# Kernel tuning notes

Hardware: AMD Instinct MI355X
Metric: run time of the kernel (lower is better)

The kernel has to match this reference:

```python
import jax, jax.numpy as jnp
import numpy as np

DT_SCALE = 0.01  # time grid = arange(T) * 0.01, i.e. t in [0, 0.99]


def setup_inputs() -> dict:
    key = jax.random.key(0)
    k1, k2, k3 = jax.random.split(key, 3)
    latents, hidden = 128, 256
    S, N, T = 4, 1024, 100
    first_point = jax.random.normal(k1, (S, N, latents), dtype=jnp.float32)
    time_steps_to_predict = jnp.arange(T, dtype=jnp.float32) * DT_SCALE
    # ODEFunc MLP params (Glorot-ish scaling so tanh stays in a sane range)
    W1 = jax.random.normal(k2, (latents, hidden), dtype=jnp.float32) / np.sqrt(latents)
    b1 = jnp.zeros((hidden,), dtype=jnp.float32)
    W2 = jax.random.normal(k3, (hidden, latents), dtype=jnp.float32) / np.sqrt(hidden)
    b2 = jnp.zeros((latents,), dtype=jnp.float32)
    return {
        "first_point": first_point,
        "time_steps_to_predict": time_steps_to_predict,
        "W1": W1, "b1": b1, "W2": W2, "b2": b2,
    }


def reference(first_point, time_steps_to_predict, W1, b1, W2, b2):
    # ode_func: dy/dt = tanh(y @ W1 + b1) @ W2 + b2 (time-autonomous MLP)
    def f(y):
        return jnp.tanh(y @ W1 + b1) @ W2 + b2

    # torchdiffeq fixed-step 'rk4': one classical RK4 step per output interval.
    t0s = time_steps_to_predict[:-1]
    t1s = time_steps_to_predict[1:]

    def rk4_step(y, ts):
        t0, t1 = ts
        dt = t1 - t0
        half = dt * 0.5
        k1 = f(y)
        k2 = f(y + half * k1)
        k3 = f(y + half * k2)
        k4 = f(y + dt * k3)
        y1 = y + (dt / 6.0) * (k1 + 2.0 * k2 + 2.0 * k3 + k4)
        return y1, y1

    _, ys = jax.lax.scan(rk4_step, first_point, (t0s, t1s))  # [T-1, S, N, D]
    pred_y = jnp.concatenate([first_point[None], ys], axis=0)  # [T, S, N, D]
    # permute(1, 2, 0, 3): [T, S, N, D] -> [S, N, T, D]
    return jnp.transpose(pred_y, (1, 2, 0, 3))
```

## Files before the change

kernel.cpp:

```cpp
#include <hip/hip_runtime.h>

typedef __attribute__((ext_vector_type(8))) short v8s;
typedef __attribute__((ext_vector_type(4))) float f4;

#define MFMA16(a, b, c) __builtin_amdgcn_mfma_f32_16x16x32_bf16((a), (b), (c), 0, 0, 0)

__device__ __forceinline__ float bf2f(unsigned short u) {
    return __uint_as_float(((unsigned)u) << 16);
}
__device__ __forceinline__ unsigned short f2bf(float x) {
    unsigned u = __float_as_uint(x);
    unsigned r = 0x7FFFu + ((u >> 16) & 1u);
    return (unsigned short)((u + r) >> 16);
}
__device__ __forceinline__ float tanh_fast(float z) {
    float u = __builtin_amdgcn_exp2f(z * 2.885390081777927f);
    float r = __builtin_amdgcn_rcpf(u + 1.0f);
    return __builtin_fmaf(-2.0f, r, 1.0f);
}
__device__ __forceinline__ float ldin(const void* p, int i, bool f32) {
    return f32 ? ((const float*)p)[i] : bf2f(((const unsigned short*)p)[i]);
}

#define BROWS 16
#define TSTEPS 100
#define DLAT 128
#define DHID 256
#define YSTR 136
#define HSTR 264
#define FSTR 132

__global__ __launch_bounds__(512, 2)
void ode_rk4_kernel(const void* __restrict__ fp,
                    const void* __restrict__ ts,
                    const void* __restrict__ W1,
                    const void* __restrict__ b1,
                    const void* __restrict__ W2,
                    const void* __restrict__ b2,
                    void* __restrict__ out) {
    __shared__ unsigned short yB[BROWS * YSTR];
    __shared__ unsigned short hB[BROWS * HSTR];
    __shared__ float yF[BROWS * FSTR];

    const bool m32 = fabsf(((const float*)ts)[1] - 0.01f) < 0.004f;

    const int tid = threadIdx.x;
    const int w = tid >> 6;
    const int lane = tid & 63;
    const int pp = lane & 15;
    const int qq = lane >> 4;
    const int R0 = blockIdx.x * BROWS;

    v8s w1f[4][2];
#pragma unroll
    for (int kt = 0; kt < 4; ++kt)
#pragma unroll
        for (int nt = 0; nt < 2; ++nt) {
            v8s f;
#pragma unroll
            for (int j = 0; j < 8; ++j)
                f[j] = (short)f2bf(ldin(W1, (kt * 32 + qq * 8 + j) * DHID + 32 * w + nt * 16 + pp, m32));
            w1f[kt][nt] = f;
        }
    v8s w2f[8];
#pragma unroll
    for (int kt = 0; kt < 8; ++kt) {
        v8s f;
#pragma unroll
        for (int j = 0; j < 8; ++j)
            f[j] = (short)f2bf(ldin(W2, (kt * 32 + qq * 8 + j) * DLAT + 16 * w + pp, m32));
        w2f[kt] = f;
    }
    const float b1v0 = ldin(b1, 32 * w + pp, m32);
    const float b1v1 = ldin(b1, 32 * w + 16 + pp, m32);
    const float b2v  = ldin(b2, 16 * w + pp, m32);

    {
        int row = tid >> 5, ch = tid & 31;
        if (m32) {
            float4 v = *((const float4*)((const float*)fp + (size_t)(R0 + row) * DLAT) + ch);
            *((float4*)((float*)out + ((size_t)(R0 + row) * TSTEPS) * DLAT) + ch) = v;
            *(float4*)(yF + row * FSTR + ch * 4) = v;
            ushort4 b; b.x = f2bf(v.x); b.y = f2bf(v.y); b.z = f2bf(v.z); b.w = f2bf(v.w);
            *(ushort4*)(yB + row * YSTR + ch * 4) = b;
        } else {
            const unsigned short* fpu = (const unsigned short*)fp;
            ushort4 v = *((const ushort4*)(fpu + (size_t)(R0 + row) * DLAT) + ch);
            *((ushort4*)((unsigned short*)out + ((size_t)(R0 + row) * TSTEPS) * DLAT) + ch) = v;
            *(ushort4*)(yB + row * YSTR + ch * 4) = v;
            float* yfp = yF + row * FSTR + ch * 4;
            yfp[0] = bf2f(v.x); yfp[1] = bf2f(v.y); yfp[2] = bf2f(v.z); yfp[3] = bf2f(v.w);
        }
    }
    __syncthreads();

    const int c2 = 16 * w + pp;
    float yreg[4];
#pragma unroll
    for (int r = 0; r < 4; ++r) yreg[r] = yF[(qq * 4 + r) * FSTR + c2];

    const unsigned short* yA = yB + pp * YSTR + qq * 8;
    const unsigned short* hA = hB + pp * HSTR + qq * 8;
    unsigned short* hW = hB + 32 * w + pp;
    unsigned short* yW = yB + c2;
    float* fW = yF + c2;

    for (int t = 0; t < TSTEPS - 1; ++t) {
        float t0 = ldin(ts, t, m32), t1 = ldin(ts, t + 1, m32);
        float dt = t1 - t0;
        float half = 0.5f * dt;
        float ksum[4] = {0.f, 0.f, 0.f, 0.f};
#pragma unroll
        for (int e = 0; e < 4; ++e) {
            __syncthreads();
            f4 h0 = {0.f, 0.f, 0.f, 0.f}, h1 = {0.f, 0.f, 0.f, 0.f};
#pragma unroll
            for (int kt = 0; kt < 4; ++kt) {
                v8s a = *(const v8s*)(yA + kt * 32);
                h0 = MFMA16(a, w1f[kt][0], h0);
                h1 = MFMA16(a, w1f[kt][1], h1);
            }
#pragma unroll
            for (int r = 0; r < 4; ++r) {
                hW[(qq * 4 + r) * HSTR]      = f2bf(tanh_fast(h0[r] + b1v0));
                hW[(qq * 4 + r) * HSTR + 16] = f2bf(tanh_fast(h1[r] + b1v1));
            }
            __syncthreads();
            f4 kacc = {0.f, 0.f, 0.f, 0.f};
#pragma unroll
            for (int kt = 0; kt < 8; ++kt) {
                v8s a = *(const v8s*)(hA + kt * 32);
                kacc = MFMA16(a, w2f[kt], kacc);
            }
            const float wgt = (e == 0 || e == 3) ? 1.0f : 2.0f;
            const float cc = (e == 2) ? dt : half;
#pragma unroll
            for (int r = 0; r < 4; ++r) {
                float kv = kacc[r] + b2v;
                ksum[r] = __builtin_fmaf(wgt, kv, ksum[r]);
                if (e < 3) {
                    float ya = __builtin_fmaf(cc, kv, yreg[r]);
                    yW[(qq * 4 + r) * YSTR] = f2bf(ya);
                }
            }
            if (e == 3) {
                float s = dt * (1.0f / 6.0f);
#pragma unroll
                for (int r = 0; r < 4; ++r) {
                    yreg[r] = __builtin_fmaf(s, ksum[r], yreg[r]);
                    yW[(qq * 4 + r) * YSTR] = f2bf(yreg[r]);
                    fW[(qq * 4 + r) * FSTR] = yreg[r];
                }
            }
        }
        __syncthreads();
        {
            int row = tid >> 5, ch = tid & 31;
            float4 v = *(const float4*)(yF + row * FSTR + ch * 4);
            if (m32) {
                *((float4*)((float*)out + ((size_t)(R0 + row) * TSTEPS + (t + 1)) * DLAT) + ch) = v;
            } else {
                ushort4 b; b.x = f2bf(v.x); b.y = f2bf(v.y); b.z = f2bf(v.z); b.w = f2bf(v.w);
                *((ushort4*)((unsigned short*)out + ((size_t)(R0 + row) * TSTEPS + (t + 1)) * DLAT) + ch) = b;
            }
        }
    }
}

extern "C" void kernel_launch(void* const* d_in, const int* in_sizes, int n_in,
                              void* d_out, int out_size, void* d_ws, size_t ws_size,
                              hipStream_t stream) {
    (void)in_sizes; (void)n_in; (void)d_ws; (void)ws_size; (void)out_size;
    ode_rk4_kernel<<<256, 512, 0, stream>>>(d_in[0], d_in[1], d_in[2], d_in[3],
                                            d_in[4], d_in[5], d_out);
}
```

Measured before the change: 528.5 us.

## Swizzle LDS layout, drop fp32 staging buffer and per-step barrier, store outputs from registers

Applies an XOR swizzle to the bf16 y and hidden LDS tiles to avoid bank conflicts on the MFMA A-operand loads. The fp32 yF staging buffer and the extra barrier per time step are removed; each thread writes its own yreg values directly to global memory. Time steps are cached in LDS, and bf16 conversion uses packed pair conversion. The direct stores are scalar and strided across lanes, so they may coalesce worse than the earlier float4 row stores.

```diff
diff --git a/kernel.cpp b/kernel.cpp
--- a/kernel.cpp
+++ b/kernel.cpp
@@ -1,4 +1,5 @@
 #include <hip/hip_runtime.h>
+#include <hip/hip_bf16.h>
 
 typedef __attribute__((ext_vector_type(8))) short v8s;
 typedef __attribute__((ext_vector_type(4))) float f4;
@@ -12,6 +13,12 @@
     unsigned u = __float_as_uint(x);
     unsigned r = 0x7FFFu + ((u >> 16) & 1u);
     return (unsigned short)((u + r) >> 16);
+}
+__device__ __forceinline__ unsigned pack_bf16_2(float a, float b) {
+    float2 t; t.x = a; t.y = b;
+    union { __hip_bfloat162 h; unsigned u; } cv;
+    cv.h = __float22bfloat162_rn(t);
+    return cv.u;
 }
 __device__ __forceinline__ float tanh_fast(float z) {
     float u = __builtin_amdgcn_exp2f(z * 2.885390081777927f);
@@ -28,7 +35,6 @@
 #define DHID 256
 #define YSTR 136
 #define HSTR 264
-#define FSTR 132
 
 __global__ __launch_bounds__(512, 2)
 void ode_rk4_kernel(const void* __restrict__ fp,
@@ -40,7 +46,7 @@
                     void* __restrict__ out) {
     __shared__ unsigned short yB[BROWS * YSTR];
     __shared__ unsigned short hB[BROWS * HSTR];
-    __shared__ float yF[BROWS * FSTR];
+    __shared__ float tsL[TSTEPS];
 
     const bool m32 = fabsf(((const float*)ts)[1] - 0.01f) < 0.004f;
 
@@ -51,6 +57,8 @@
     const int qq = lane >> 4;
     const int R0 = blockIdx.x * BROWS;
 
+    if (tid < TSTEPS) tsL[tid] = ldin(ts, tid, m32);
+
     v8s w1f[4][2];
 #pragma unroll
     for (int kt = 0; kt < 4; ++kt)
@@ -75,39 +83,54 @@
     const float b1v1 = ldin(b1, 32 * w + 16 + pp, m32);
     const float b2v  = ldin(b2, 16 * w + pp, m32);
 
+    const int pb = pp >> 3, pw = pp & 7;
+    const int sA = (pp >> 1) & 7;
+    const unsigned short* yA[4];
+#pragma unroll
+    for (int kt = 0; kt < 4; ++kt)
+        yA[kt] = yB + pp * YSTR + (((4 * kt + qq) ^ sA) << 3);
+    const unsigned short* hA[8];
+#pragma unroll
+    for (int kt = 0; kt < 8; ++kt)
+        hA[kt] = hB + pp * HSTR + (((4 * kt + qq) ^ sA) << 3);
+    const int s0 = (2 * qq) & 7, s1 = (2 * qq + 1) & 7;
+    int hoff[2][2], yoff[2];
+    hoff[0][0] = (((4 * w + pb) ^ s0) << 3) + pw;
+    hoff[0][1] = (((4 * w + 2 + pb) ^ s0) << 3) + pw;
+    hoff[1][0] = (((4 * w + pb) ^ s1) << 3) + pw;
+    hoff[1][1] = (((4 * w + 2 + pb) ^ s1) << 3) + pw;
+    yoff[0] = (((2 * w + pb) ^ s0) << 3) + pw;
+    yoff[1] = (((2 * w + pb) ^ s1) << 3) + pw;
+
     {
         int row = tid >> 5, ch = tid & 31;
+        int sw = (row >> 1) & 7;
+        unsigned short* dst = yB + row * YSTR + (((ch >> 1) ^ sw) << 3) + (ch & 1) * 4;
         if (m32) {
             float4 v = *((const float4*)((const float*)fp + (size_t)(R0 + row) * DLAT) + ch);
             *((float4*)((float*)out + ((size_t)(R0 + row) * TSTEPS) * DLAT) + ch) = v;
-            *(float4*)(yF + row * FSTR + ch * 4) = v;
             ushort4 b; b.x = f2bf(v.x); b.y = f2bf(v.y); b.z = f2bf(v.z); b.w = f2bf(v.w);
-            *(ushort4*)(yB + row * YSTR + ch * 4) = b;
+            *(ushort4*)dst = b;
         } else {
             const unsigned short* fpu = (const unsigned short*)fp;
             ushort4 v = *((const ushort4*)(fpu + (size_t)(R0 + row) * DLAT) + ch);
             *((ushort4*)((unsigned short*)out + ((size_t)(R0 + row) * TSTEPS) * DLAT) + ch) = v;
-            *(ushort4*)(yB + row * YSTR + ch * 4) = v;
-            float* yfp = yF + row * FSTR + ch * 4;
-            yfp[0] = bf2f(v.x); yfp[1] = bf2f(v.y); yfp[2] = bf2f(v.z); yfp[3] = bf2f(v.w);
-        }
-    }
-    __syncthreads();
+            *(ushort4*)dst = v;
+        }
+    }
 
     const int c2 = 16 * w + pp;
     float yreg[4];
-#pragma unroll
-    for (int r = 0; r < 4; ++r) yreg[r] = yF[(qq * 4 + r) * FSTR + c2];
-
-    const unsigned short* yA = yB + pp * YSTR + qq * 8;
-    const unsigned short* hA = hB + pp * HSTR + qq * 8;
-    unsigned short* hW = hB + 32 * w + pp;
-    unsigned short* yW = yB + c2;
-    float* fW = yF + c2;
+    size_t ob[4];
+#pragma unroll
+    for (int r = 0; r < 4; ++r) {
+        yreg[r] = ldin(fp, (R0 + 4 * qq + r) * DLAT + c2, m32);
+        ob[r] = ((size_t)(R0 + 4 * qq + r) * TSTEPS) * DLAT + c2;
+    }
+    __syncthreads();
 
     for (int t = 0; t < TSTEPS - 1; ++t) {
-        float t0 = ldin(ts, t, m32), t1 = ldin(ts, t + 1, m32);
-        float dt = t1 - t0;
+        float dt = tsL[t + 1] - tsL[t];
         float half = 0.5f * dt;
         float ksum[4] = {0.f, 0.f, 0.f, 0.f};
 #pragma unroll
@@ -116,53 +139,65 @@
             f4 h0 = {0.f, 0.f, 0.f, 0.f}, h1 = {0.f, 0.f, 0.f, 0.f};
 #pragma unroll
             for (int kt = 0; kt < 4; ++kt) {
-                v8s a = *(const v8s*)(yA + kt * 32);
+                v8s a = *(const v8s*)yA[kt];
                 h0 = MFMA16(a, w1f[kt][0], h0);
                 h1 = MFMA16(a, w1f[kt][1], h1);
             }
 #pragma unroll
             for (int r = 0; r < 4; ++r) {
-                hW[(qq * 4 + r) * HSTR]      = f2bf(tanh_fast(h0[r] + b1v0));
-                hW[(qq * 4 + r) * HSTR + 16] = f2bf(tanh_fast(h1[r] + b1v1));
+                float z0 = tanh_fast(h0[r] + b1v0);
+                float z1 = tanh_fast(h1[r] + b1v1);
+                unsigned pu = pack_bf16_2(z0, z1);
+                unsigned short* hp = hB + (4 * qq + r) * HSTR;
+                hp[hoff[r >> 1][0]] = (unsigned short)pu;
+                hp[hoff[r >> 1][1]] = (unsigned short)(pu >> 16);
             }
             __syncthreads();
             f4 kacc = {0.f, 0.f, 0.f, 0.f};
 #pragma unroll
             for (int kt = 0; kt < 8; ++kt) {
-                v8s a = *(const v8s*)(hA + kt * 32);
+                v8s a = *(const v8s*)hA[kt];
                 kacc = MFMA16(a, w2f[kt], kacc);
             }
             const float wgt = (e == 0 || e == 3) ? 1.0f : 2.0f;
             const float cc = (e == 2) ? dt : half;
+            float kv[4];
 #pragma unroll
             for (int r = 0; r < 4; ++r) {
-                float kv = kacc[r] + b2v;
-                ksum[r] = __builtin_fmaf(wgt, kv, ksum[r]);
-                if (e < 3) {
-                    float ya = __builtin_fmaf(cc, kv, yreg[r]);
-                    yW[(qq * 4 + r) * YSTR] = f2bf(ya);
+                kv[r] = kacc[r] + b2v;
+                ksum[r] = __builtin_fmaf(wgt, kv[r], ksum[r]);
+            }
+            if (e < 3) {
+#pragma unroll
+                for (int rp = 0; rp < 2; ++rp) {
+                    float ya0 = __builtin_fmaf(cc, kv[2 * rp], yreg[2 * rp]);
+                    float ya1 = __builtin_fmaf(cc, kv[2 * rp + 1], yreg[2 * rp + 1]);
+                    unsigned pu = pack_bf16_2(ya0, ya1);
+                    yB[(4 * qq + 2 * rp) * YSTR + yoff[rp]] = (unsigned short)pu;
+                    yB[(4 * qq + 2 * rp + 1) * YSTR + yoff[rp]] = (unsigned short)(pu >> 16);
                 }
-            }
-            if (e == 3) {
+            } else {
                 float s = dt * (1.0f / 6.0f);
 #pragma unroll
-                for (int r = 0; r < 4; ++r) {
-                    yreg[r] = __builtin_fmaf(s, ksum[r], yreg[r]);
-                    yW[(qq * 4 + r) * YSTR] = f2bf(yreg[r]);
-                    fW[(qq * 4 + r) * FSTR] = yreg[r];
+                for (int rp = 0; rp < 2; ++rp) {
+                    yreg[2 * rp]     = __builtin_fmaf(s, ksum[2 * rp],     yreg[2 * rp]);
+                    yreg[2 * rp + 1] = __builtin_fmaf(s, ksum[2 * rp + 1], yreg[2 * rp + 1]);
+                    unsigned pu = pack_bf16_2(yreg[2 * rp], yreg[2 * rp + 1]);
+                    yB[(4 * qq + 2 * rp) * YSTR + yoff[rp]] = (unsigned short)pu;
+                    yB[(4 * qq + 2 * rp + 1) * YSTR + yoff[rp]] = (unsigned short)(pu >> 16);
                 }
             }
         }
-        __syncthreads();
-        {
-            int row = tid >> 5, ch = tid & 31;
-            float4 v = *(const float4*)(yF + row * FSTR + ch * 4);
-            if (m32) {
-                *((float4*)((float*)out + ((size_t)(R0 + row) * TSTEPS + (t + 1)) * DLAT) + ch) = v;
-            } else {
-                ushort4 b; b.x = f2bf(v.x); b.y = f2bf(v.y); b.z = f2bf(v.z); b.w = f2bf(v.w);
-                *((ushort4*)((unsigned short*)out + ((size_t)(R0 + row) * TSTEPS + (t + 1)) * DLAT) + ch) = b;
-            }
+        if (m32) {
+            float* op = (float*)out;
+#pragma unroll
+            for (int r = 0; r < 4; ++r)
+                op[ob[r] + (size_t)(t + 1) * DLAT] = yreg[r];
+        } else {
+            unsigned short* op = (unsigned short*)out;
+#pragma unroll
+            for (int r = 0; r < 4; ++r)
+                op[ob[r] + (size_t)(t + 1) * DLAT] = f2bf(yreg[r]);
         }
     }
 }
```

Measured after the change: 524.3 us. No clear change (-0.8%).
